# Performance work log

Measured on AMD Instinct MI355X. Metric: run time of the kernel, lower is better.

The kernel has to match this reference:

```python
import jax, jax.numpy as jnp
import numpy as np

ALPHA = 1.0   # stored by the module but unused in forward
SPLIT = 4
FILTER = 2


def _resize_bilinear(x, out_h, out_w):
    """PyTorch F.interpolate(mode='bilinear', align_corners=False), no antialias.
    x: [B, C, H, W]."""
    B, C, H, W = x.shape

    def coords(out_n, in_n):
        c = (jnp.arange(out_n, dtype=jnp.float32) + 0.5) * (in_n / out_n) - 0.5
        c = jnp.clip(c, 0.0, in_n - 1)
        i0 = jnp.floor(c).astype(jnp.int32)
        i1 = jnp.minimum(i0 + 1, in_n - 1)
        f = (c - i0).astype(x.dtype)
        return i0, i1, f

    r0, r1, fr = coords(out_h, H)
    c0, c1, fc = coords(out_w, W)
    # separable: rows then cols
    x = x[:, :, r0, :] * (1 - fr)[None, None, :, None] + x[:, :, r1, :] * fr[None, None, :, None]
    x = x[:, :, :, c0] * (1 - fc) + x[:, :, :, c1] * fc
    return x


def setup_inputs() -> dict:
    key = jax.random.key(0)
    targets = jax.random.normal(key, (8, 3, 2560, 2560), dtype=jnp.float32)
    return {"targets": targets}


def reference(targets):
    B, C, H, W = targets.shape
    s = SPLIT
    h = int(H / s / 10)
    w = int(W / s / 10)
    x = _resize_bilinear(targets, h * s, w * s)  # [B, C, s*h, s*w]

    # The original quadruple loop over shifts (i,j) and patches (n,m) computes, for
    # every ordered patch pair (a=(n,m), b=((n+i)%s,(m+j)%s)),
    #   map[a, b] = mean_{B,C,h,w} exp(-(patch_b - patch_a)^2),
    # which is exactly the full pairwise patch-affinity matrix.
    P = x.reshape(B, C, s, h, s, w).transpose(2, 4, 0, 1, 3, 5).reshape(s * s, -1)  # [s^2, D]
    aff = jnp.exp(-(P[:, None, :] - P[None, :, :]) ** 2).mean(axis=-1)  # [s^2, s^2]

    # Sort-based masking: zero the (split - filter) smallest entries of each row.
    k = s - FILTER
    idx = jnp.argsort(aff, axis=1)[:, :k]           # [s^2, k]
    rows = jnp.arange(s * s)[:, None]
    aff = aff.at[rows, idx].set(0.0)
    return aff
```

## Files before the change

kernel.cpp:

```cpp
#include <hip/hip_runtime.h>


#define W_IN 2560
#define IMG_STRIDE (2560 * 2560)
#define D_TOTAL_I 98304
#define D_TOTAL 98304.0

#define NSHADOW 16
#define SLOT_STRIDE 128
#define SHADOW_BYTES (NSHADOW * SLOT_STRIDE * 8)
#define PMAT_OFF 65536
#define WS_NEEDED (PMAT_OFF + 16 * D_TOTAL_I * 4)


__global__ __launch_bounds__(256) void pm_resize_stream(const float* __restrict__ in,
                                                        float* __restrict__ Pm,
                                                        unsigned int* __restrict__ wsu) {
    const int blk = blockIdx.x;
    const int tid = threadIdx.x;

    if (blk < 16) wsu[blk * 256 + tid] = 0u;

    const int i   = blk & 255;
    const int img = blk >> 8;

    __shared__ float rows[2 * W_IN];
    const float4* s4 = reinterpret_cast<const float4*>(
        in + (size_t)img * IMG_STRIDE + (size_t)(10 * i + 4) * W_IN);
    float4* l4 = reinterpret_cast<float4*>(rows);
#pragma unroll
    for (int q = 0; q < 5; ++q) l4[q * 256 + tid] = s4[q * 256 + tid];
    __syncthreads();

    const int j = tid;
    float a = rows[10 * j + 4], b = rows[10 * j + 5];
    float c = rows[W_IN + 10 * j + 4], d = rows[W_IN + 10 * j + 5];
    const int n = i >> 6, hh = i & 63;
    const int m = j >> 6, ww = j & 63;
    Pm[(size_t)(n * 4 + m) * D_TOTAL_I + img * 4096 + hh * 64 + ww] =
        0.25f * ((a + b) + (c + d));
}


template <int HALF>
__device__ __forceinline__ void pm_fill(const float* __restrict__ P,
                                        float* __restrict__ v) {
    int k = 0;
#pragma unroll
    for (int a = 0; a < 16; ++a)
#pragma unroll
        for (int b = a + 1; b < 16; ++b) {
            if (k >= HALF * 60 && k < HALF * 60 + 60) {
                float df = P[a] - P[b];
                v[k - HALF * 60] = __expf(-df * df);
            }
            ++k;
        }
}

__global__ __launch_bounds__(256) void pm_pairs(const float* __restrict__ Pm,
                                                double* __restrict__ acc) {
    const int tid  = threadIdx.x;
    const int lane = tid & 63;
    const int half = tid >> 7;
    const int d    = blockIdx.x * 128 + (tid & 127);

    float P[16];
#pragma unroll
    for (int p = 0; p < 16; ++p) P[p] = Pm[p * D_TOTAL_I + d];

    float v[64];
    if (half == 0) pm_fill<0>(P, v);
    else           pm_fill<1>(P, v);
    v[60] = 0.0f; v[61] = 0.0f; v[62] = 0.0f; v[63] = 0.0f;

#define PM_STAGE(K, H)                                         \
    {                                                          \
        const bool bit = (lane >> (K)) & 1;                    \
        _Pragma("unroll")                                      \
        for (int i = 0; i < (H); ++i) {                        \
            float keep = bit ? v[i + (H)] : v[i];              \
            float send = bit ? v[i] : v[i + (H)];              \
            v[i] = keep + __shfl_xor(send, 1 << (K), 64);      \
        }                                                      \
    }
    PM_STAGE(0, 32)
    PM_STAGE(1, 16)
    PM_STAGE(2, 8)
    PM_STAGE(3, 4)
    PM_STAGE(4, 2)
    PM_STAGE(5, 1)
#undef PM_STAGE

    const int r = __brev(lane) >> 26;
    double* shadow = acc + (size_t)(blockIdx.x & (NSHADOW - 1)) * SLOT_STRIDE;
    if (r < 60) atomicAdd(&shadow[half * 64 + r], (double)v[0]);
}


__global__ __launch_bounds__(256) void pm_finish(const double* __restrict__ acc,
                                                 float* __restrict__ out) {
    __shared__ float aff[256];
    const int tid = threadIdx.x;
    const int a = tid >> 4, b = tid & 15;
    if (a < b) {
        const int k = 15 * a - (a * (a - 1)) / 2 + (b - a - 1);
        const int slot = (k < 60) ? k : k + 4;
        double s = 0.0;
#pragma unroll
        for (int c = 0; c < NSHADOW; ++c) s += acc[c * SLOT_STRIDE + slot];
        float vv = (float)(s * (1.0 / D_TOTAL));
        aff[a * 16 + b] = vv;
        aff[b * 16 + a] = vv;
    } else if (a == b) {
        aff[tid] = 1.0f;
    }
    __syncthreads();
    if (tid < 16) {
        const float* row = &aff[tid * 16];
        float v1 = 1e30f; int i1 = -1;
        for (int j = 0; j < 16; ++j) {
            float x = row[j];
            if (x < v1) { v1 = x; i1 = j; }
        }
        float v2 = 1e30f; int i2 = -1;
        for (int j = 0; j < 16; ++j) {
            if (j == i1) continue;
            float x = row[j];
            if (x < v2) { v2 = x; i2 = j; }
        }
        for (int j = 0; j < 16; ++j)
            out[tid * 16 + j] = (j == i1 || j == i2) ? 0.0f : row[j];
    }
}


#define NPAIR_SLOTS_FB 256
#define NSHADOW_FB 8

__global__ __launch_bounds__(64) void pm_accum_fb(const float* __restrict__ in,
                                                  double* __restrict__ acc) {
    const int blk = blockIdx.x;
    const int hh  = blk & 63;
    const int img = blk >> 6;
    const int ww  = threadIdx.x;

    const float* base = in + (size_t)img * IMG_STRIDE;
    float P[16];
#pragma unroll
    for (int n = 0; n < 4; ++n) {
        const float* r0 = base + (size_t)(10 * (n * 64 + hh) + 4) * W_IN;
#pragma unroll
        for (int m = 0; m < 4; ++m) {
            const int col = 10 * (m * 64 + ww) + 4;
            float2 t = *reinterpret_cast<const float2*>(r0 + col);
            float2 u = *reinterpret_cast<const float2*>(r0 + W_IN + col);
            P[n * 4 + m] = 0.25f * ((t.x + t.y) + (u.x + u.y));
        }
    }
    double* shadow = acc + (size_t)(blk & (NSHADOW_FB - 1)) * NPAIR_SLOTS_FB;
    int k = 0;
#pragma unroll
    for (int a = 0; a < 16; ++a)
#pragma unroll
        for (int b = a + 1; b < 16; ++b) {
            float dd = P[a] - P[b];
            float vv = __expf(-dd * dd);
#pragma unroll
            for (int s = 32; s >= 1; s >>= 1) vv += __shfl_xor(vv, s, 64);
            if (ww == (k & 63)) atomicAdd(&shadow[a * 16 + b], (double)vv);
            ++k;
        }
}

__global__ __launch_bounds__(256) void pm_finish_fb(const double* __restrict__ acc,
                                                    float* __restrict__ out) {
    __shared__ float aff[256];
    const int tid = threadIdx.x;
    const int a = tid >> 4, b = tid & 15;
    if (a < b) {
        double s = 0.0;
#pragma unroll
        for (int c = 0; c < NSHADOW_FB; ++c) s += acc[c * NPAIR_SLOTS_FB + tid];
        float vv = (float)(s * (1.0 / D_TOTAL));
        aff[a * 16 + b] = vv;
        aff[b * 16 + a] = vv;
    } else if (a == b) {
        aff[tid] = 1.0f;
    }
    __syncthreads();
    if (tid < 16) {
        const float* row = &aff[tid * 16];
        float v1 = 1e30f; int i1 = -1;
        for (int j = 0; j < 16; ++j) {
            float x = row[j];
            if (x < v1) { v1 = x; i1 = j; }
        }
        float v2 = 1e30f; int i2 = -1;
        for (int j = 0; j < 16; ++j) {
            if (j == i1) continue;
            float x = row[j];
            if (x < v2) { v2 = x; i2 = j; }
        }
        for (int j = 0; j < 16; ++j)
            out[tid * 16 + j] = (j == i1 || j == i2) ? 0.0f : row[j];
    }
}


extern "C" void kernel_launch(void* const* d_in, const int* in_sizes, int n_in,
                              void* d_out, int out_size, void* d_ws, size_t ws_size,
                              hipStream_t stream) {
    const float* in = (const float*)d_in[0];
    float* out = (float*)d_out;

    if (ws_size >= (size_t)WS_NEEDED) {
        double* acc = (double*)d_ws;
        unsigned int* wsu = (unsigned int*)d_ws;
        float* Pm = (float*)((char*)d_ws + PMAT_OFF);
        pm_resize_stream<<<dim3(6144), dim3(256), 0, stream>>>(in, Pm, wsu);
        pm_pairs<<<dim3(768), dim3(256), 0, stream>>>(Pm, acc);
        pm_finish<<<dim3(1), dim3(256), 0, stream>>>(acc, out);
    } else {
        double* acc = (double*)d_ws;
        hipMemsetAsync(d_ws, 0, NSHADOW_FB * NPAIR_SLOTS_FB * sizeof(double), stream);
        pm_accum_fb<<<dim3(1536), dim3(64), 0, stream>>>(in, acc);
        pm_finish_fb<<<dim3(1), dim3(256), 0, stream>>>(acc, out);
    }
}
```

Baseline: 32.75 us.

## Process three row-pairs per block with register prefetch of the next pair

The resize kernel now handles three row-pairs per block, launching 2048 blocks instead of 6144. While the current pair is reduced out of shared memory, the next pair is loaded into registers, overlapping global loads with compute. This cuts block launch overhead and hides load latency. The cost is fewer blocks in flight, more registers per thread and an extra barrier per iteration. The result depends on whether the kernel is bound by memory latency or by bandwidth.

Result: slower. 56.46 us (+72.4%).

```diff
diff --git a/kernel.cpp b/kernel.cpp
--- a/kernel.cpp
+++ b/kernel.cpp
@@ -13,32 +13,55 @@
 #define WS_NEEDED (PMAT_OFF + 16 * D_TOTAL_I * 4)
 
 
-__global__ __launch_bounds__(256) void pm_resize_stream(const float* __restrict__ in,
-                                                        float* __restrict__ Pm,
-                                                        unsigned int* __restrict__ wsu) {
+__global__ __launch_bounds__(256) void pm_resize_pipe(const float* __restrict__ in,
+                                                      float* __restrict__ Pm,
+                                                      unsigned int* __restrict__ wsu) {
     const int blk = blockIdx.x;
     const int tid = threadIdx.x;
 
     if (blk < 16) wsu[blk * 256 + tid] = 0u;
 
-    const int i   = blk & 255;
-    const int img = blk >> 8;
-
     __shared__ float rows[2 * W_IN];
-    const float4* s4 = reinterpret_cast<const float4*>(
-        in + (size_t)img * IMG_STRIDE + (size_t)(10 * i + 4) * W_IN);
-    float4* l4 = reinterpret_cast<float4*>(rows);
-#pragma unroll
-    for (int q = 0; q < 5; ++q) l4[q * 256 + tid] = s4[q * 256 + tid];
-    __syncthreads();
-
-    const int j = tid;
-    float a = rows[10 * j + 4], b = rows[10 * j + 5];
-    float c = rows[W_IN + 10 * j + 4], d = rows[W_IN + 10 * j + 5];
-    const int n = i >> 6, hh = i & 63;
-    const int m = j >> 6, ww = j & 63;
-    Pm[(size_t)(n * 4 + m) * D_TOTAL_I + img * 4096 + hh * 64 + ww] =
-        0.25f * ((a + b) + (c + d));
+
+    float4 reg[5];
+    {
+        const int c = blk * 3;
+        const int i = c & 255, img = c >> 8;
+        const float4* s4 = reinterpret_cast<const float4*>(
+            in + (size_t)img * IMG_STRIDE + (size_t)(10 * i + 4) * W_IN);
+#pragma unroll
+        for (int q = 0; q < 5; ++q) reg[q] = s4[q * 256 + tid];
+    }
+
+#pragma unroll
+    for (int g = 0; g < 3; ++g) {
+        float4* l4 = reinterpret_cast<float4*>(rows);
+#pragma unroll
+        for (int q = 0; q < 5; ++q) l4[q * 256 + tid] = reg[q];
+        __syncthreads();
+
+        if (g < 2) {
+            const int c = blk * 3 + g + 1;
+            const int i = c & 255, img = c >> 8;
+            const float4* s4 = reinterpret_cast<const float4*>(
+                in + (size_t)img * IMG_STRIDE + (size_t)(10 * i + 4) * W_IN);
+#pragma unroll
+            for (int q = 0; q < 5; ++q) reg[q] = s4[q * 256 + tid];
+        }
+
+        {
+            const int c = blk * 3 + g;
+            const int i = c & 255, img = c >> 8;
+            const int j = tid;
+            float a = rows[10 * j + 4],        b = rows[10 * j + 5];
+            float e = rows[W_IN + 10 * j + 4], f = rows[W_IN + 10 * j + 5];
+            const int n = i >> 6, hh = i & 63;
+            const int m = j >> 6, ww = j & 63;
+            Pm[(size_t)(n * 4 + m) * D_TOTAL_I + img * 4096 + hh * 64 + ww] =
+                0.25f * ((a + b) + (e + f));
+        }
+        if (g < 2) __syncthreads();
+    }
 }
 
 
@@ -218,7 +241,7 @@
         double* acc = (double*)d_ws;
         unsigned int* wsu = (unsigned int*)d_ws;
         float* Pm = (float*)((char*)d_ws + PMAT_OFF);
-        pm_resize_stream<<<dim3(6144), dim3(256), 0, stream>>>(in, Pm, wsu);
+        pm_resize_pipe<<<dim3(2048), dim3(256), 0, stream>>>(in, Pm, wsu);
         pm_pairs<<<dim3(768), dim3(256), 0, stream>>>(Pm, acc);
         pm_finish<<<dim3(1), dim3(256), 0, stream>>>(acc, out);
     } else {
```
